# Kernel optimization log

Hardware: AMD Instinct MI355X
Metric: run time of the kernel (lower is better)

Reference implementation:

```python
import jax, jax.numpy as jnp
import numpy as np

H = 7    # hidden dim
IN = 5   # input features
B = 8192
T = 512


def setup_inputs() -> dict:
    key = jax.random.key(0)
    ks = jax.random.split(key, 10)
    s = 1.0 / np.sqrt(H)  # torch default uniform bound for GRU/Linear
    u = lambda k, shape, b: jax.random.uniform(k, shape, jnp.float32, -b, b)
    return {
        "x": jax.random.normal(ks[0], (B, T, IN), dtype=jnp.float32),
        "batch_size": B,
        # GRU weights (torch layout: gates stacked [r; z; n] along dim 0)
        "W_ih": u(ks[1], (3 * H, IN), s),
        "W_hh": u(ks[2], (3 * H, H), s),
        "b_ih": u(ks[3], (3 * H,), s),
        "b_hh": u(ks[4], (3 * H,), s),
        # h0 = Linear(1, H, bias=False) applied to constant 1 -> weight column
        "W_h0": u(ks[5], (H, 1), 1.0),
        # output heads
        "W_m": u(ks[6], (3, H), s),
        "b_m": u(ks[7], (3,), s),
        "W_r": u(ks[8], (1, H), s),
        "b_r": u(ks[9], (1,), s),
    }


def reference(x, batch_size, W_ih, W_hh, b_ih, b_hh, W_h0, W_m, b_m, W_r, b_r):
    h_dim = W_hh.shape[1]
    # h_init = self.h0(ones(batch,1)) -> broadcast weight column  [B, H]
    h0 = jnp.broadcast_to(W_h0[:, 0], (batch_size, h_dim))
    # precompute input projection for all timesteps: [B, T, 3H]
    xp = jnp.einsum('bti,gi->btg', x, W_ih) + b_ih

    def step(h, xp_t):
        gh = h @ W_hh.T + b_hh                     # [B, 3H]
        xr, xz, xn = jnp.split(xp_t, 3, axis=-1)
        hr, hz, hn = jnp.split(gh, 3, axis=-1)
        r = jax.nn.sigmoid(xr + hr)
        z = jax.nn.sigmoid(xz + hz)
        n = jnp.tanh(xn + r * hn)
        h_new = (1.0 - z) * n + z * h
        return h_new, h_new

    h_last, all_h = jax.lax.scan(step, h0, jnp.swapaxes(xp, 0, 1))
    all_h = jnp.swapaxes(all_h, 0, 1)              # [B, T, H]
    # per-sample Linear heads in the original loop == one batched matmul
    out_m = all_h @ W_m.T + b_m                    # [B, T, 3]
    out_r = all_h @ W_r.T + b_r                    # [B, T, 1]
    return out_m, out_r, h_last[None]              # h_last: [1, B, H]
```

## Files before the change

### kernel.cpp

```cpp
#include <hip/hip_runtime.h>


namespace {
constexpr int Bn = 8192;
constexpr int Tn = 512;
constexpr int INn = 5;
constexpr int Hn = 7;
constexpr int TILE = 32;
constexpr int NTILE = Tn / TILE;
constexpr int BPB = 16;
constexpr int XSTR = 164;
constexpr long long OFF_OR = (long long)Bn * Tn * 3;
constexpr long long OFF_HL = OFF_OR + (long long)Bn * Tn;
constexpr float LOG2E = 1.44269504088896340736f;
}

typedef float v2f __attribute__((ext_vector_type(2)));

__device__ __forceinline__ v2f pk_fma(v2f a, v2f b, v2f c) {
    return __builtin_elementwise_fma(a, b, c);
}
__device__ __forceinline__ v2f splat2(float x) { return (v2f){x, x}; }

__device__ __forceinline__ float fast_sigmoid(float x) {
    float e = __builtin_amdgcn_exp2f(-LOG2E * x);
    return __builtin_amdgcn_rcpf(1.0f + e);
}
__device__ __forceinline__ float fast_tanh(float x) {
    float e = __builtin_amdgcn_exp2f(-2.0f * LOG2E * x);
    return __builtin_amdgcn_rcpf(1.0f + e) * 2.0f - 1.0f;
}

template<int CTRL>
__device__ __forceinline__ float dppf(float v) {
    int r = __builtin_amdgcn_update_dpp(0, __builtin_bit_cast(int, v),
                                        CTRL, 0xF, 0xF, true);
    return __builtin_bit_cast(float, r);
}

__global__ __launch_bounds__(256, 2) void gru_fused_kernel(
    const float* __restrict__ x,
    const float* __restrict__ W_ih,
    const float* __restrict__ W_hh,
    const float* __restrict__ b_ih,
    const float* __restrict__ b_hh,
    const float* __restrict__ W_h0,
    const float* __restrict__ W_m,
    const float* __restrict__ b_m,
    const float* __restrict__ W_r,
    const float* __restrict__ b_r,
    float* __restrict__ out)
{
    __shared__ float lds_x[2][BPB * XSTR];

    const int tid  = threadIdx.x;
    const int l    = tid & 15;
    const int j    = l & 7;
    const int g    = tid >> 4;
    const int b    = blockIdx.x * BPB + g;
    const int jj   = (j < 7) ? j : 6;
    const bool lo8 = ((l & 8) == 0);
    const bool hl  = (j == 7);

    const int row0 = lo8 ? jj : (Hn + jj);
    const int row1 = 2 * Hn + jj;

    v2f whh_rot[8];
    #pragma unroll
    for (int i = 0; i < 8; ++i) {
        const int k = (j - i) & 7;
        if (k < 7) {
            if (hl) {
                const float w0 = lo8 ? W_m[0 * Hn + k] : W_m[2 * Hn + k];
                const float w1 = lo8 ? W_m[1 * Hn + k] : W_r[k];
                whh_rot[i] = (v2f){w0, w1};
            } else {
                whh_rot[i] = (v2f){W_hh[row0 * Hn + k], W_hh[row1 * Hn + k]};
            }
        } else {
            whh_rot[i] = (v2f){0.0f, 0.0f};
        }
    }
    v2f wih01[INn];
    #pragma unroll
    for (int i = 0; i < INn; ++i)
        wih01[i] = hl ? (v2f){0.0f, 0.0f}
                      : (v2f){W_ih[row0 * INn + i], W_ih[row1 * INn + i]};
    const v2f biasH = hl ? (lo8 ? (v2f){b_m[0], b_m[1]}
                                : (v2f){b_m[2], b_r[0]})
                         : (v2f){b_hh[row0], b_hh[row1]};
    const v2f biasP = hl ? (v2f){0.0f, 0.0f}
                         : (v2f){b_ih[row0], b_ih[row1]};

    float hj = W_h0[jj];

    const float* xb = x + (long long)b * (Tn * INn);
    float* om  = out + (long long)b * (Tn * 3);
    float* orr = out + OFF_OR + (long long)b * Tn;

    float* hp0 = om - 3 + (lo8 ? 0 : 2);
    float* hp1 = lo8 ? (om - 2) : (orr - 1);
    const int hs1 = lo8 ? 3 : 1;

    float2 stage[5];
    #pragma unroll
    for (int i = 0; i < 5; ++i)
        stage[i] = *(const float2*)(xb + 2 * (l + 16 * i));

    int cur = 0;
    for (int tl = 0; tl < NTILE; ++tl) {
        #pragma unroll
        for (int i = 0; i < 5; ++i)
            *(float2*)&lds_x[cur][g * XSTR + 2 * (l + 16 * i)] = stage[i];
        __syncthreads();

        if (tl + 1 < NTILE) {
            const float* src = xb + (tl + 1) * (TILE * INn);
            #pragma unroll
            for (int i = 0; i < 5; ++i)
                stage[i] = *(const float2*)(src + 2 * (l + 16 * i));
        }

        const float4* xq = (const float4*)&lds_x[cur][g * XSTR];
        float4 xbuf[2][5];
        #pragma unroll
        for (int k = 0; k < 5; ++k) xbuf[0][k] = xq[k];

        #pragma unroll
        for (int c = 0; c < 8; ++c) {
            if (c < 7) {
                #pragma unroll
                for (int k = 0; k < 5; ++k)
                    xbuf[(c + 1) & 1][k] = xq[(c + 1) * 5 + k];
            }
            const float* xcf = (const float*)xbuf[c & 1];

            #pragma unroll
            for (int ss = 0; ss < 4; ++ss) {
                const int tt = c * 4 + ss;

                v2f accA = biasH;
                v2f accB = (v2f){0.0f, 0.0f};
                accA = pk_fma(whh_rot[0], splat2(hj), accA);
                {
                    float h1 = dppf<0x121>(hj);
                    accB = pk_fma(whh_rot[1], splat2(h1), accB);
                    float h2 = dppf<0x122>(hj);
                    accA = pk_fma(whh_rot[2], splat2(h2), accA);
                    float h3 = dppf<0x123>(hj);
                    accB = pk_fma(whh_rot[3], splat2(h3), accB);
                    float h4 = dppf<0x124>(hj);
                    accA = pk_fma(whh_rot[4], splat2(h4), accA);
                    float h5 = dppf<0x125>(hj);
                    accB = pk_fma(whh_rot[5], splat2(h5), accB);
                    float h6 = dppf<0x126>(hj);
                    accA = pk_fma(whh_rot[6], splat2(h6), accA);
                    float h7 = dppf<0x127>(hj);
                    accB = pk_fma(whh_rot[7], splat2(h7), accB);
                }
                v2f accH = accA + accB;

                v2f accP = biasP;
                #pragma unroll
                for (int i = 0; i < INn; ++i)
                    accP = pk_fma(wih01[i], splat2(xcf[5 * ss + i]), accP);

                if ((tl > 0 || tt > 0) && hl) {
                    *hp0 = accH[0];
                    *hp1 = accH[1];
                }
                hp0 += 3;
                hp1 += hs1;

                float s  = fast_sigmoid(accH[0] + accP[0]);
                float sv = dppf<0x128>(s);
                float r_val = lo8 ? s : sv;
                float z_val = lo8 ? sv : s;
                float n = fast_tanh(fmaf(r_val, accH[1], accP[1]));
                hj = n + z_val * (hj - n);
            }
        }
        cur ^= 1;
    }

    {
        v2f accA = biasH;
        v2f accB = (v2f){0.0f, 0.0f};
        accA = pk_fma(whh_rot[0], splat2(hj), accA);
        accB = pk_fma(whh_rot[1], splat2(dppf<0x121>(hj)), accB);
        accA = pk_fma(whh_rot[2], splat2(dppf<0x122>(hj)), accA);
        accB = pk_fma(whh_rot[3], splat2(dppf<0x123>(hj)), accB);
        accA = pk_fma(whh_rot[4], splat2(dppf<0x124>(hj)), accA);
        accB = pk_fma(whh_rot[5], splat2(dppf<0x125>(hj)), accB);
        accA = pk_fma(whh_rot[6], splat2(dppf<0x126>(hj)), accA);
        accB = pk_fma(whh_rot[7], splat2(dppf<0x127>(hj)), accB);
        v2f accH = accA + accB;
        if (hl) {
            *hp0 = accH[0];
            *hp1 = accH[1];
        }
    }

    if (l < Hn) out[OFF_HL + (long long)b * Hn + l] = hj;
}

extern "C" void kernel_launch(void* const* d_in, const int* in_sizes, int n_in,
                              void* d_out, int out_size, void* d_ws, size_t ws_size,
                              hipStream_t stream) {
    const float* x    = (const float*)d_in[0];
    const float* W_ih = (const float*)d_in[2];
    const float* W_hh = (const float*)d_in[3];
    const float* b_ih = (const float*)d_in[4];
    const float* b_hh = (const float*)d_in[5];
    const float* W_h0 = (const float*)d_in[6];
    const float* W_m  = (const float*)d_in[7];
    const float* b_m  = (const float*)d_in[8];
    const float* W_r  = (const float*)d_in[9];
    const float* b_r  = (const float*)d_in[10];
    float* out = (float*)d_out;

    dim3 grid(Bn / BPB);
    dim3 block(256);
    gru_fused_kernel<<<grid, block, 0, stream>>>(x, W_ih, W_hh, b_ih, b_hh,
                                                 W_h0, W_m, b_m, W_r, b_r, out);
}
```

Baseline: 234.1 us.

## Map each sample to 8 lanes and stage outputs in LDS for coalesced stores

Each batch sample now uses 8 lanes instead of 16, so every lane computes the r, z and n gates for one hidden unit. This removes the cross-half DPP exchange of the sigmoid result. The log2e and activation constants are folded into the weights and biases ahead of time, which removes multiplies from the per-step critical path. Head outputs are written to a per-sample LDS ring and flushed once per 16-step tile as contiguous stores, replacing scattered per-step global writes. Blocks now hold 32 samples and the launch bound drops to one block per CU, which lowers occupancy and raises per-lane work; latency hiding may suffer as a result.

```diff
diff --git a/kernel.cpp b/kernel.cpp
--- a/kernel.cpp
+++ b/kernel.cpp
@@ -6,10 +6,12 @@
 constexpr int Tn = 512;
 constexpr int INn = 5;
 constexpr int Hn = 7;
-constexpr int TILE = 32;
+constexpr int TILE = 16;
 constexpr int NTILE = Tn / TILE;
-constexpr int BPB = 16;
-constexpr int XSTR = 164;
+constexpr int CPT = 4;
+constexpr int BPB = 32;
+constexpr int XSTR = 84;
+constexpr int RSTR = 140;
 constexpr long long OFF_OR = (long long)Bn * Tn * 3;
 constexpr long long OFF_HL = OFF_OR + (long long)Bn * Tn;
 constexpr float LOG2E = 1.44269504088896340736f;
@@ -21,15 +23,6 @@
     return __builtin_elementwise_fma(a, b, c);
 }
 __device__ __forceinline__ v2f splat2(float x) { return (v2f){x, x}; }
-
-__device__ __forceinline__ float fast_sigmoid(float x) {
-    float e = __builtin_amdgcn_exp2f(-LOG2E * x);
-    return __builtin_amdgcn_rcpf(1.0f + e);
-}
-__device__ __forceinline__ float fast_tanh(float x) {
-    float e = __builtin_amdgcn_exp2f(-2.0f * LOG2E * x);
-    return __builtin_amdgcn_rcpf(1.0f + e) * 2.0f - 1.0f;
-}
 
 template<int CTRL>
 __device__ __forceinline__ float dppf(float v) {
@@ -38,7 +31,7 @@
     return __builtin_bit_cast(float, r);
 }
 
-__global__ __launch_bounds__(256, 2) void gru_fused_kernel(
+__global__ __launch_bounds__(256, 1) void gru_fused_kernel(
     const float* __restrict__ x,
     const float* __restrict__ W_ih,
     const float* __restrict__ W_hh,
@@ -52,83 +45,107 @@
     float* __restrict__ out)
 {
     __shared__ float lds_x[2][BPB * XSTR];
+    __shared__ float lds_r[BPB * RSTR];
 
     const int tid  = threadIdx.x;
     const int l    = tid & 15;
     const int j    = l & 7;
     const int g    = tid >> 4;
-    const int b    = blockIdx.x * BPB + g;
-    const int jj   = (j < 7) ? j : 6;
-    const bool lo8 = ((l & 8) == 0);
-    const bool hl  = (j == 7);
-
-    const int row0 = lo8 ? jj : (Hn + jj);
-    const int row1 = 2 * Hn + jj;
-
-    v2f whh_rot[8];
+    const int sm   = tid >> 3;
+    const int b    = blockIdx.x * BPB + sm;
+    const bool pad = (j == 7);
+
+    const float kR = -LOG2E;
+    const float kN = -2.0f * LOG2E;
+
+    v2f  wrz[8];
+    float wn[8];
     #pragma unroll
     for (int i = 0; i < 8; ++i) {
         const int k = (j - i) & 7;
         if (k < 7) {
-            if (hl) {
-                const float w0 = lo8 ? W_m[0 * Hn + k] : W_m[2 * Hn + k];
-                const float w1 = lo8 ? W_m[1 * Hn + k] : W_r[k];
-                whh_rot[i] = (v2f){w0, w1};
+            if (pad) {
+                wrz[i] = (v2f){W_m[0 * Hn + k], W_m[1 * Hn + k]};
+                wn[i]  = W_m[2 * Hn + k];
             } else {
-                whh_rot[i] = (v2f){W_hh[row0 * Hn + k], W_hh[row1 * Hn + k]};
+                wrz[i] = (v2f){kR * W_hh[j * Hn + k],
+                               kR * W_hh[(Hn + j) * Hn + k]};
+                wn[i]  = kN * W_hh[(2 * Hn + j) * Hn + k];
             }
         } else {
-            whh_rot[i] = (v2f){0.0f, 0.0f};
-        }
-    }
-    v2f wih01[INn];
-    #pragma unroll
-    for (int i = 0; i < INn; ++i)
-        wih01[i] = hl ? (v2f){0.0f, 0.0f}
-                      : (v2f){W_ih[row0 * INn + i], W_ih[row1 * INn + i]};
-    const v2f biasH = hl ? (lo8 ? (v2f){b_m[0], b_m[1]}
-                                : (v2f){b_m[2], b_r[0]})
-                         : (v2f){b_hh[row0], b_hh[row1]};
-    const v2f biasP = hl ? (v2f){0.0f, 0.0f}
-                         : (v2f){b_ih[row0], b_ih[row1]};
-
-    float hj = W_h0[jj];
+            wrz[i] = (v2f){0.0f, 0.0f};
+            wn[i]  = 0.0f;
+        }
+    }
+    v2f  wpx[INn];
+    float wpn[INn];
+    #pragma unroll
+    for (int i = 0; i < INn; ++i) {
+        wpx[i] = pad ? (v2f){0.0f, 0.0f}
+                     : (v2f){kR * W_ih[j * INn + i],
+                             kR * W_ih[(Hn + j) * INn + i]};
+        wpn[i] = pad ? 0.0f : kN * W_ih[(2 * Hn + j) * INn + i];
+    }
+    const v2f biasRZ = pad ? (v2f){b_m[0], b_m[1]}
+                           : (v2f){kR * (b_ih[j] + b_hh[j]),
+                                   kR * (b_ih[Hn + j] + b_hh[Hn + j])};
+    const float biasNh = pad ? b_m[2] : kN * b_hh[2 * Hn + j];
+    const float biasNx = pad ? 0.0f   : kN * b_ih[2 * Hn + j];
+    const float wrl = (j < Hn) ? W_r[j] : 0.0f;
+    const float brv = b_r[0];
+
+    const bool ge1 = (j >= 1), ge2 = (j >= 2), ge3 = (j >= 3), ge4 = (j >= 4),
+               ge5 = (j >= 5), ge6 = (j >= 6), ge7 = (j >= 7);
+
+    float hj = W_h0[(j < Hn) ? j : 6];
 
     const float* xb = x + (long long)b * (Tn * INn);
     float* om  = out + (long long)b * (Tn * 3);
     float* orr = out + OFF_OR + (long long)b * Tn;
-
-    float* hp0 = om - 3 + (lo8 ? 0 : 2);
-    float* hp1 = lo8 ? (om - 2) : (orr - 1);
-    const int hs1 = lo8 ? 3 : 1;
+    float* ring = &lds_r[sm * RSTR];
+
+    int fq[3];
+    #pragma unroll
+    for (int i = 0; i < 3; ++i) {
+        const int q = i * 16 + l;
+        fq[i] = (q % 3) * 40 + q / 3;
+    }
+    const float* ringA = &lds_r[(2 * g) * RSTR];
+    const float* ringB = &lds_r[(2 * g + 1) * RSTR];
+    float* omA = out + (long long)(blockIdx.x * BPB + 2 * g) * (Tn * 3);
+    float* omB = omA + Tn * 3;
+    float* orA = out + OFF_OR + (long long)(blockIdx.x * BPB + 2 * g) * Tn;
+    float* orB = orA + Tn;
+
+    const int u = tid & 7;
 
     float2 stage[5];
     #pragma unroll
     for (int i = 0; i < 5; ++i)
-        stage[i] = *(const float2*)(xb + 2 * (l + 16 * i));
+        stage[i] = *(const float2*)(xb + 2 * (u + 8 * i));
 
     int cur = 0;
     for (int tl = 0; tl < NTILE; ++tl) {
         #pragma unroll
         for (int i = 0; i < 5; ++i)
-            *(float2*)&lds_x[cur][g * XSTR + 2 * (l + 16 * i)] = stage[i];
+            *(float2*)&lds_x[cur][sm * XSTR + 2 * (u + 8 * i)] = stage[i];
         __syncthreads();
 
         if (tl + 1 < NTILE) {
             const float* src = xb + (tl + 1) * (TILE * INn);
             #pragma unroll
             for (int i = 0; i < 5; ++i)
-                stage[i] = *(const float2*)(src + 2 * (l + 16 * i));
-        }
-
-        const float4* xq = (const float4*)&lds_x[cur][g * XSTR];
+                stage[i] = *(const float2*)(src + 2 * (u + 8 * i));
+        }
+
+        const float4* xq = (const float4*)&lds_x[cur][sm * XSTR];
         float4 xbuf[2][5];
         #pragma unroll
         for (int k = 0; k < 5; ++k) xbuf[0][k] = xq[k];
 
         #pragma unroll
-        for (int c = 0; c < 8; ++c) {
-            if (c < 7) {
+        for (int c = 0; c < CPT; ++c) {
+            if (c + 1 < CPT) {
                 #pragma unroll
                 for (int k = 0; k < 5; ++k)
                     xbuf[(c + 1) & 1][k] = xq[(c + 1) * 5 + k];
@@ -139,69 +156,122 @@
             for (int ss = 0; ss < 4; ++ss) {
                 const int tt = c * 4 + ss;
 
-                v2f accA = biasH;
-                v2f accB = (v2f){0.0f, 0.0f};
-                accA = pk_fma(whh_rot[0], splat2(hj), accA);
+                v2f aczA = biasRZ, aczB = (v2f){0.0f, 0.0f};
+                float anA = biasNh, anB = 0.0f;
+                aczA = pk_fma(wrz[0], splat2(hj), aczA);
+                anA  = fmaf(wn[0], hj, anA);
+                #define ROT(i, GE, CA, CB, ACZ, AN)                        \
+                {                                                          \
+                    float ra = dppf<CA>(hj);                               \
+                    float rb = dppf<CB>(hj);                               \
+                    float hv = GE ? ra : rb;                               \
+                    ACZ = pk_fma(wrz[i], splat2(hv), ACZ);                 \
+                    AN  = fmaf(wn[i], hv, AN);                             \
+                }
+                ROT(1, ge1, 0x121, 0x129, aczB, anB)
+                ROT(2, ge2, 0x122, 0x12A, aczA, anA)
+                ROT(3, ge3, 0x123, 0x12B, aczB, anB)
+                ROT(4, ge4, 0x124, 0x12C, aczA, anA)
+                ROT(5, ge5, 0x125, 0x12D, aczB, anB)
+                ROT(6, ge6, 0x126, 0x12E, aczA, anA)
+                ROT(7, ge7, 0x127, 0x12F, aczB, anB)
+                #undef ROT
+                v2f acz = aczA + aczB;
+                float an = anA + anB;
+
+                v2f pxy = (v2f){0.0f, 0.0f};
+                float pn = biasNx;
+                #pragma unroll
+                for (int i = 0; i < INn; ++i) {
+                    pxy = pk_fma(wpx[i], splat2(xcf[5 * ss + i]), pxy);
+                    pn  = fmaf(wpn[i], xcf[5 * ss + i], pn);
+                }
+
+                float rr = wrl * hj;
+                rr += dppf<0xB1>(rr);
+                rr += dppf<0x4E>(rr);
+                rr += dppf<0x141>(rr);
+                if (pad) {
+                    ring[tt]      = acz[0];
+                    ring[40 + tt] = acz[1];
+                }
                 {
-                    float h1 = dppf<0x121>(hj);
-                    accB = pk_fma(whh_rot[1], splat2(h1), accB);
-                    float h2 = dppf<0x122>(hj);
-                    accA = pk_fma(whh_rot[2], splat2(h2), accA);
-                    float h3 = dppf<0x123>(hj);
-                    accB = pk_fma(whh_rot[3], splat2(h3), accB);
-                    float h4 = dppf<0x124>(hj);
-                    accA = pk_fma(whh_rot[4], splat2(h4), accA);
-                    float h5 = dppf<0x125>(hj);
-                    accB = pk_fma(whh_rot[5], splat2(h5), accB);
-                    float h6 = dppf<0x126>(hj);
-                    accA = pk_fma(whh_rot[6], splat2(h6), accA);
-                    float h7 = dppf<0x127>(hj);
-                    accB = pk_fma(whh_rot[7], splat2(h7), accB);
-                }
-                v2f accH = accA + accB;
-
-                v2f accP = biasP;
-                #pragma unroll
-                for (int i = 0; i < INn; ++i)
-                    accP = pk_fma(wih01[i], splat2(xcf[5 * ss + i]), accP);
-
-                if ((tl > 0 || tt > 0) && hl) {
-                    *hp0 = accH[0];
-                    *hp1 = accH[1];
-                }
-                hp0 += 3;
-                hp1 += hs1;
-
-                float s  = fast_sigmoid(accH[0] + accP[0]);
-                float sv = dppf<0x128>(s);
-                float r_val = lo8 ? s : sv;
-                float z_val = lo8 ? sv : s;
-                float n = fast_tanh(fmaf(r_val, accH[1], accP[1]));
-                hj = n + z_val * (hj - n);
+                    const bool w = pad || (j == 0);
+                    float v = pad ? an : (rr + brv);
+                    if (w) ring[(pad ? 80 : 120) + tt] = v;
+                }
+
+                v2f pre = acz + pxy;
+                float er = __builtin_amdgcn_exp2f(pre[0]);
+                float ez = __builtin_amdgcn_exp2f(pre[1]);
+                float sr = __builtin_amdgcn_rcpf(1.0f + er);
+                float sz = __builtin_amdgcn_rcpf(1.0f + ez);
+                float pnf = fmaf(sr, an, pn);
+                float et = __builtin_amdgcn_exp2f(pnf);
+                float t  = __builtin_amdgcn_rcpf(1.0f + et);
+                float n  = fmaf(2.0f, t, -1.0f);
+                hj = fmaf(sz, hj - n, n);
+            }
+        }
+
+        {
+            float* omtA = omA + tl * 48 - 3;
+            float* omtB = omB + tl * 48 - 3;
+            #pragma unroll
+            for (int i = 0; i < 3; ++i) {
+                float vA = ringA[fq[i]];
+                float vB = ringB[fq[i]];
+                if (tl > 0 || i > 0 || l >= 3) {
+                    omtA[i * 16 + l] = vA;
+                    omtB[i * 16 + l] = vB;
+                }
+            }
+            float rA = ringA[120 + l];
+            float rB = ringB[120 + l];
+            if (tl > 0 || l > 0) {
+                orA[tl * 16 - 1 + l] = rA;
+                orB[tl * 16 - 1 + l] = rB;
             }
         }
         cur ^= 1;
     }
 
     {
-        v2f accA = biasH;
-        v2f accB = (v2f){0.0f, 0.0f};
-        accA = pk_fma(whh_rot[0], splat2(hj), accA);
-        accB = pk_fma(whh_rot[1], splat2(dppf<0x121>(hj)), accB);
-        accA = pk_fma(whh_rot[2], splat2(dppf<0x122>(hj)), accA);
-        accB = pk_fma(whh_rot[3], splat2(dppf<0x123>(hj)), accB);
-        accA = pk_fma(whh_rot[4], splat2(dppf<0x124>(hj)), accA);
-        accB = pk_fma(whh_rot[5], splat2(dppf<0x125>(hj)), accB);
-        accA = pk_fma(whh_rot[6], splat2(dppf<0x126>(hj)), accA);
-        accB = pk_fma(whh_rot[7], splat2(dppf<0x127>(hj)), accB);
-        v2f accH = accA + accB;
-        if (hl) {
-            *hp0 = accH[0];
-            *hp1 = accH[1];
-        }
-    }
-
-    if (l < Hn) out[OFF_HL + (long long)b * Hn + l] = hj;
+        v2f aczA = biasRZ, aczB = (v2f){0.0f, 0.0f};
+        float anA = biasNh, anB = 0.0f;
+        aczA = pk_fma(wrz[0], splat2(hj), aczA);
+        anA  = fmaf(wn[0], hj, anA);
+        #define ROT(i, GE, CA, CB, ACZ, AN)                        \
+        {                                                          \
+            float ra = dppf<CA>(hj);                               \
+            float rb = dppf<CB>(hj);                               \
+            float hv = GE ? ra : rb;                               \
+            ACZ = pk_fma(wrz[i], splat2(hv), ACZ);                 \
+            AN  = fmaf(wn[i], hv, AN);                             \
+        }
+        ROT(1, ge1, 0x121, 0x129, aczB, anB)
+        ROT(2, ge2, 0x122, 0x12A, aczA, anA)
+        ROT(3, ge3, 0x123, 0x12B, aczB, anB)
+        ROT(4, ge4, 0x124, 0x12C, aczA, anA)
+        ROT(5, ge5, 0x125, 0x12D, aczB, anB)
+        ROT(6, ge6, 0x126, 0x12E, aczA, anA)
+        ROT(7, ge7, 0x127, 0x12F, aczB, anB)
+        #undef ROT
+        v2f acz = aczA + aczB;
+        float an = anA + anB;
+        float rr = wrl * hj;
+        rr += dppf<0xB1>(rr);
+        rr += dppf<0x4E>(rr);
+        rr += dppf<0x141>(rr);
+        if (pad) {
+            om[(Tn - 1) * 3 + 0] = acz[0];
+            om[(Tn - 1) * 3 + 1] = acz[1];
+            om[(Tn - 1) * 3 + 2] = an;
+        }
+        if (j == 0) orr[Tn - 1] = rr + brv;
+    }
+
+    if (j < Hn) out[OFF_HL + (long long)b * Hn + j] = hj;
 }
 
 extern "C" void kernel_launch(void* const* d_in, const int* in_sizes, int n_in,
```

New measurement: 242.9 us. +3.8%, slower.
